# Optimization experiments

Measured on AMD Instinct MI355X. Metric: run time of the kernel, lower is better.

The kernel has to match this reference:

```python
import jax, jax.numpy as jnp
import numpy as np

N = 50000      # nodes
E = 800000     # edges (before self-loops)
H = 1          # attention heads
C = 64         # hidden channels per head
G = 256        # graphs in batch
IN = 1         # input_channel
NEG_SLOPE = 0.2
BN_EPS = 1e-5


def setup_inputs() -> dict:
    key = jax.random.key(0)
    ks = jax.random.split(key, 16)
    X = jax.random.normal(ks[0], (N, IN), dtype=jnp.float32)
    edge_index = jax.random.randint(ks[1], (2, E), 0, N, dtype=jnp.int32)
    batch = jnp.sort(jax.random.randint(ks[2], (N,), 0, G, dtype=jnp.int32))
    # GATConv params: conv1 maps IN -> H*C, conv2..5 map H*C -> H*C
    W1 = jax.random.normal(ks[3], (IN, H * C), dtype=jnp.float32) * 0.1
    Ws = jax.random.normal(ks[4], (4, H * C, H * C), dtype=jnp.float32) * 0.05
    att_src = jax.random.normal(ks[5], (5, H, C), dtype=jnp.float32) * 0.1
    att_dst = jax.random.normal(ks[6], (5, H, C), dtype=jnp.float32) * 0.1
    bias = jnp.zeros((5, H * C), dtype=jnp.float32)
    # BatchNorm1d (eval mode) params per layer
    bn_gamma = 1.0 + 0.1 * jax.random.normal(ks[7], (5, H * C), dtype=jnp.float32)
    bn_beta = 0.1 * jax.random.normal(ks[8], (5, H * C), dtype=jnp.float32)
    bn_mean = 0.1 * jax.random.normal(ks[9], (5, H * C), dtype=jnp.float32)
    bn_var = jax.random.uniform(ks[10], (5, H * C), dtype=jnp.float32, minval=0.5, maxval=1.5)
    Wr = jax.random.normal(ks[11], (H * C, 1), dtype=jnp.float32) * 0.1
    br = jnp.zeros((1,), dtype=jnp.float32)
    return {"X": X, "edge_index": edge_index, "batch": batch, "W1": W1, "Ws": Ws,
            "att_src": att_src, "att_dst": att_dst, "bias": bias,
            "bn_gamma": bn_gamma, "bn_beta": bn_beta, "bn_mean": bn_mean,
            "bn_var": bn_var, "Wr": Wr, "br": br}


def _gat_layer(x, src, dst, W, a_s, a_d, b):
    # x: [N, Fin]; src/dst: [E+N] (self-loops included)
    h = (x @ W).reshape(N, H, C)                        # [N,H,C]
    alpha_src = jnp.sum(h * a_s, axis=-1)               # [N,H]
    alpha_dst = jnp.sum(h * a_d, axis=-1)               # [N,H]
    e = jax.nn.leaky_relu(alpha_src[src] + alpha_dst[dst], NEG_SLOPE)  # [E+N,H]
    m = jax.ops.segment_max(e, dst, num_segments=N)     # per-dst softmax (stable)
    w = jnp.exp(e - m[dst])
    z = jax.ops.segment_sum(w, dst, num_segments=N)
    alpha = w / z[dst]                                  # [E+N,H]
    out = jax.ops.segment_sum(h[src] * alpha[..., None], dst, num_segments=N)
    return out.reshape(N, H * C) + b


def reference(X, edge_index, batch, W1, Ws, att_src, att_dst, bias,
              bn_gamma, bn_beta, bn_mean, bn_var, Wr, br):
    loops = jnp.arange(N, dtype=edge_index.dtype)
    src = jnp.concatenate([edge_index[0], loops])       # PyG GATConv adds self-loops
    dst = jnp.concatenate([edge_index[1], loops])

    def bn(x, i):
        return (x - bn_mean[i]) * (bn_gamma[i] / jnp.sqrt(bn_var[i] + BN_EPS)) + bn_beta[i]

    x = bn(jax.nn.relu(_gat_layer(X, src, dst, W1, att_src[0], att_dst[0], bias[0])), 0)
    for i in range(4):  # conv2..conv5 (dropout is identity in eval)
        x = bn(jax.nn.relu(_gat_layer(x, src, dst, Ws[i], att_src[i + 1], att_dst[i + 1], bias[i + 1])), i + 1)

    counts = jax.ops.segment_sum(jnp.ones((N,), x.dtype), batch, num_segments=G)
    pooled = jax.ops.segment_sum(x, batch, num_segments=G) / jnp.maximum(counts, 1.0)[:, None]
    pred = pooled @ Wr + br                             # [G,1]
    return pred, pooled
```

## Files before the change

### kernel.cpp

```cpp
#include <hip/hip_runtime.h>
#include <hip/hip_fp16.h>
#include <math.h>


#define CH   4096
#define BCAP 8192

__global__ __launch_bounds__(256) void bucket_scatter_kernel(const int* __restrict__ esrc,
                                                             const int* __restrict__ edst,
                                                             int* __restrict__ bkt_cursor,
                                                             unsigned* __restrict__ ebuf,
                                                             int E, int N, int NB) {
    __shared__ unsigned buf[CH];
    __shared__ unsigned short bkt[CH];
    __shared__ int histA[256], base[256], curB[256], gofs[256];
    int t    = threadIdx.x;
    int T    = E + N;
    int c0   = blockIdx.x * CH;
    int cend = min(c0 + CH, T);
    int M    = cend - c0;
    histA[t] = 0;
    __syncthreads();
    for (int i = c0 + t; i < cend; i += 256) {
        int d = (i < E) ? edst[i] : (i - E);
        atomicAdd(&histA[d >> 8], 1);
    }
    __syncthreads();
    int v = histA[t];
    base[t] = v;
    __syncthreads();
    for (int o = 1; o < 256; o <<= 1) {
        int u = (t >= o) ? base[t - o] : 0;
        __syncthreads();
        base[t] += u;
        __syncthreads();
    }
    int excl = base[t] - v;
    __syncthreads();
    base[t] = excl;
    curB[t] = excl;
    __syncthreads();
    if (t < NB && v > 0)
        gofs[t] = t * BCAP + atomicAdd(&bkt_cursor[t], v);
    for (int i = c0 + t; i < cend; i += 256) {
        int s, d;
        if (i < E) { s = esrc[i]; d = edst[i]; }
        else       { s = i - E;   d = s; }
        int b = d >> 8;
        int r = atomicAdd(&curB[b], 1);
        buf[r] = ((unsigned)s << 8) | (unsigned)(d & 255);
        bkt[r] = (unsigned short)b;
    }
    __syncthreads();
    for (int i = t; i < M; i += 256) {
        int b = bkt[i];
        ebuf[gofs[b] + (i - base[b])] = buf[i];
    }
}

__global__ __launch_bounds__(256) void bucket_sort_kernel(const unsigned* __restrict__ ebuf,
                                                          const int* __restrict__ bkt_cursor,
                                                          int* __restrict__ row_start,
                                                          int* __restrict__ csr_src, int N, int NB) {
    __shared__ int cnt[256], ofs[256];
    __shared__ int csr_lds[BCAP];
    int t    = threadIdx.x;
    int b    = blockIdx.x;
    int n0   = b << 8;
    int n1   = min(n0 + 256, N);
    int M    = bkt_cursor[b];
    ofs[t] = (t < b) ? bkt_cursor[t] : 0;
    __syncthreads();
    for (int o = 1; o < 256; o <<= 1) {
        int u = (t >= o) ? ofs[t - o] : 0;
        __syncthreads();
        ofs[t] += u;
        __syncthreads();
    }
    int base = ofs[255];
    __syncthreads();
    const unsigned* reg = ebuf + (size_t)b * BCAP;
    cnt[t] = 0;
    __syncthreads();
    for (int i = t; i < M; i += 256) atomicAdd(&cnt[reg[i] & 255u], 1);
    __syncthreads();
    int v = cnt[t];
    ofs[t] = v;
    __syncthreads();
    for (int o = 1; o < 256; o <<= 1) {
        int u = (t >= o) ? ofs[t - o] : 0;
        __syncthreads();
        ofs[t] += u;
        __syncthreads();
    }
    int excl = ofs[t] - v;
    if (n0 + t < n1) row_start[n0 + t] = base + excl;
    if (b == NB - 1 && t == 0) row_start[N] = base + M;
    __syncthreads();
    cnt[t] = excl;
    __syncthreads();
    for (int i = t; i < M; i += 256) {
        unsigned e = reg[i];
        int p = atomicAdd(&cnt[e & 255u], 1);
        csr_lds[p] = (int)(e >> 8);
    }
    __syncthreads();
    for (int i = t; i < M; i += 256) csr_src[base + i] = csr_lds[i];
}

__global__ __launch_bounds__(256) void aggregate1_kernel(const float* __restrict__ X,
                                                         const float* __restrict__ W1,
                                                         const float* __restrict__ a_s,
                                                         const float* __restrict__ a_d,
                                                         const int* __restrict__ row_start,
                                                         const int* __restrict__ csr_src,
                                                         const float* __restrict__ bias,
                                                         const float* __restrict__ gamma,
                                                         const float* __restrict__ beta,
                                                         const float* __restrict__ mean,
                                                         const float* __restrict__ var,
                                                         __half* __restrict__ xout, int N) {
    int lane = threadIdx.x & 63;
    int wave = threadIdx.x >> 6;
    int wpb  = blockDim.x >> 6;
    float w  = W1[lane];
    float da = w * a_s[lane];
    float db = w * a_d[lane];
#pragma unroll
    for (int o = 32; o > 0; o >>= 1) {
        da += __shfl_xor(da, o, 64);
        db += __shfl_xor(db, o, 64);
    }
    float bc    = bias[lane];
    float scale = gamma[lane] * rsqrtf(var[lane] + 1e-5f);
    float shift = beta[lane] - mean[lane] * scale;
    for (int d = blockIdx.x * wpb + wave; d < N; d += gridDim.x * wpb) {
        int rs  = row_start[d], re = row_start[d + 1];
        int deg = re - rs;
        float add = db * X[d];
        float S = 0.f, z = 0.f;
        if (deg <= 64) {
            float xs = 0.f, wj = 0.f;
            if (lane < deg) {
                xs = X[csr_src[rs + lane]];
                float e = da * xs + add;
                e  = (e > 0.f) ? e : 0.2f * e;
                wj = __expf(fminf(e, 60.f));
            }
            z = wj;
            S = wj * xs;
#pragma unroll
            for (int o = 32; o > 0; o >>= 1) {
                z += __shfl_xor(z, o, 64);
                S += __shfl_xor(S, o, 64);
            }
        } else {
            for (int j = rs + lane; j < re; j += 64) {
                float xs = X[csr_src[j]];
                float e  = da * xs + add;
                e = (e > 0.f) ? e : 0.2f * e;
                float wj = __expf(fminf(e, 60.f));
                z += wj;
                S += wj * xs;
            }
#pragma unroll
            for (int o = 32; o > 0; o >>= 1) {
                z += __shfl_xor(z, o, 64);
                S += __shfl_xor(S, o, 64);
            }
        }
        float o = w * (S / z) + bc;
        o = fmaxf(o, 0.f);
        xout[(size_t)d * 64 + lane] = __float2half(fmaf(o, scale, shift));
    }
}

__global__ __launch_bounds__(256) void transform_kernel(const __half* __restrict__ x16,
                                                        const float* __restrict__ W,
                                                        const float* __restrict__ a_s,
                                                        const float* __restrict__ a_d,
                                                        __half* __restrict__ h16,
                                                        float* __restrict__ as,
                                                        float* __restrict__ ad, int N) {
    __shared__ float Wl[64 * 64];
    __shared__ float xT[64 * 68];
    int t    = threadIdx.x;
    int lane = t & 63;
    int wv   = t >> 6;
    int base = blockIdx.x * 64;

    for (int i = t; i < 64 * 64; i += 256) Wl[i] = W[i];
#pragma unroll
    for (int r = 0; r < 16; ++r) {
        int nl = wv * 16 + r;
        int n  = base + nl;
        float v = (n < N) ? __half2float(x16[(size_t)n * 64 + lane]) : 0.f;
        xT[lane * 68 + nl] = v;
    }
    __syncthreads();

    int c0  = (t & 15) * 4;
    int nl0 = (t >> 4) * 4;
    float acc[4][4] = {{0.f}};
#pragma unroll 8
    for (int k = 0; k < 64; ++k) {
        float4 xv = *reinterpret_cast<const float4*>(&xT[k * 68 + nl0]);
        float4 wl = *reinterpret_cast<const float4*>(&Wl[k * 64 + c0]);
        acc[0][0] = fmaf(xv.x, wl.x, acc[0][0]);
        acc[0][1] = fmaf(xv.x, wl.y, acc[0][1]);
        acc[0][2] = fmaf(xv.x, wl.z, acc[0][2]);
        acc[0][3] = fmaf(xv.x, wl.w, acc[0][3]);
        acc[1][0] = fmaf(xv.y, wl.x, acc[1][0]);
        acc[1][1] = fmaf(xv.y, wl.y, acc[1][1]);
        acc[1][2] = fmaf(xv.y, wl.z, acc[1][2]);
        acc[1][3] = fmaf(xv.y, wl.w, acc[1][3]);
        acc[2][0] = fmaf(xv.z, wl.x, acc[2][0]);
        acc[2][1] = fmaf(xv.z, wl.y, acc[2][1]);
        acc[2][2] = fmaf(xv.z, wl.z, acc[2][2]);
        acc[2][3] = fmaf(xv.z, wl.w, acc[2][3]);
        acc[3][0] = fmaf(xv.w, wl.x, acc[3][0]);
        acc[3][1] = fmaf(xv.w, wl.y, acc[3][1]);
        acc[3][2] = fmaf(xv.w, wl.z, acc[3][2]);
        acc[3][3] = fmaf(xv.w, wl.w, acc[3][3]);
    }

    float4 asv = *reinterpret_cast<const float4*>(&a_s[c0]);
    float4 adv = *reinterpret_cast<const float4*>(&a_d[c0]);
#pragma unroll
    for (int i = 0; i < 4; ++i) {
        int n = base + nl0 + i;
        if (n < N) {
            union { __half2 h2[2]; uint2 u; } pk;
            pk.h2[0] = __floats2half2_rn(acc[i][0], acc[i][1]);
            pk.h2[1] = __floats2half2_rn(acc[i][2], acc[i][3]);
            *reinterpret_cast<uint2*>(&h16[(size_t)n * 64 + c0]) = pk.u;
        }
        float s1 = acc[i][0] * asv.x + acc[i][1] * asv.y + acc[i][2] * asv.z + acc[i][3] * asv.w;
        float s2 = acc[i][0] * adv.x + acc[i][1] * adv.y + acc[i][2] * adv.z + acc[i][3] * adv.w;
#pragma unroll
        for (int o = 8; o > 0; o >>= 1) {
            s1 += __shfl_xor(s1, o, 64);
            s2 += __shfl_xor(s2, o, 64);
        }
        if ((lane & 15) == 0 && n < N) { as[n] = s1; ad[n] = s2; }
    }
}

__global__ __launch_bounds__(256) void aggregate_kernel(const __half* __restrict__ h16,
                                                        const float* __restrict__ as,
                                                        const float* __restrict__ ad,
                                                        const int* __restrict__ row_start,
                                                        const int* __restrict__ csr_src,
                                                        const float* __restrict__ bias,
                                                        const float* __restrict__ gamma,
                                                        const float* __restrict__ beta,
                                                        const float* __restrict__ mean,
                                                        const float* __restrict__ var,
                                                        __half* __restrict__ xout, int N) {
    __shared__ float2 swbuf[4][64];
    int lane = threadIdx.x & 63;
    int wave = threadIdx.x >> 6;
    int wpb  = blockDim.x >> 6;
    int half = lane >> 5;
    int l    = lane & 31;
    int cg   = (l & 15) << 2;
    float4 bcv = *reinterpret_cast<const float4*>(&bias[cg]);
    float4 gav = *reinterpret_cast<const float4*>(&gamma[cg]);
    float4 bev = *reinterpret_cast<const float4*>(&beta[cg]);
    float4 mnv = *reinterpret_cast<const float4*>(&mean[cg]);
    float4 vrv = *reinterpret_cast<const float4*>(&var[cg]);
    float sc0 = gav.x * rsqrtf(vrv.x + 1e-5f), sh0 = bev.x - mnv.x * sc0;
    float sc1 = gav.y * rsqrtf(vrv.y + 1e-5f), sh1 = bev.y - mnv.y * sc1;
    float sc2 = gav.z * rsqrtf(vrv.z + 1e-5f), sh2 = bev.z - mnv.z * sc2;
    float sc3 = gav.w * rsqrtf(vrv.w + 1e-5f), sh3 = bev.w - mnv.w * sc3;
    int P = (N + 1) >> 1;
    for (int p = blockIdx.x * wpb + wave; p < P; p += gridDim.x * wpb) {
        int d0  = p << 1;
        int d1  = d0 + 1;
        int rs0 = row_start[d0];
        int re0 = row_start[d0 + 1];
        int deg0 = re0 - rs0;
        int deg1 = -1, re1 = 0;
        if (d1 < N) { re1 = row_start[d1 + 1]; deg1 = re1 - re0; }
        if (deg0 <= 32 && deg1 >= 0 && deg1 <= 32) {
            int d   = half ? d1 : d0;
            int rs  = half ? re0 : rs0;
            int deg = half ? deg1 : deg0;
            float add = ad[d];
            int s = 0; float w = 0.f;
            if (l < deg) {
                s = csr_src[rs + l];
                float e = as[s] + add;
                e = (e > 0.f) ? e : 0.2f * e;
                w = __expf(fminf(e, 60.f));
            }
            swbuf[wave][lane] = make_float2(__int_as_float(s), w);
            float z = w;
#pragma unroll
            for (int o = 16; o > 0; o >>= 1) z += __shfl_xor(z, o, 64);
            asm volatile("s_waitcnt lgkmcnt(0)" ::: "memory");
            int es = l >> 4;
            float a0 = 0.f, a1 = 0.f, a2 = 0.f, a3 = 0.f;
            int nb = (deg + 1) >> 1;
#pragma unroll 2
            for (int b = 0; b < nb; ++b) {
                int j  = (b << 1) + es;
                float2 sw = swbuf[wave][(half << 5) + j];
                int   sj = __float_as_int(sw.x);
                float wj = sw.y;
                const __half2* hp = reinterpret_cast<const __half2*>(h16 + (size_t)sj * 64 + cg);
                float2 f0 = __half22float2(hp[0]);
                float2 f1 = __half22float2(hp[1]);
                a0 = fmaf(f0.x, wj, a0);
                a1 = fmaf(f0.y, wj, a1);
                a2 = fmaf(f1.x, wj, a2);
                a3 = fmaf(f1.y, wj, a3);
            }
            a0 += __shfl_xor(a0, 16, 64);
            a1 += __shfl_xor(a1, 16, 64);
            a2 += __shfl_xor(a2, 16, 64);
            a3 += __shfl_xor(a3, 16, 64);
            if (es == 0) {
                float rz = 1.f / z;
                float o0 = fmaxf(fmaf(a0, rz, bcv.x), 0.f);
                float o1 = fmaxf(fmaf(a1, rz, bcv.y), 0.f);
                float o2 = fmaxf(fmaf(a2, rz, bcv.z), 0.f);
                float o3 = fmaxf(fmaf(a3, rz, bcv.w), 0.f);
                union { __half2 h2[2]; uint2 u; } pk;
                pk.h2[0] = __floats2half2_rn(fmaf(o0, sc0, sh0), fmaf(o1, sc1, sh1));
                pk.h2[1] = __floats2half2_rn(fmaf(o2, sc2, sh2), fmaf(o3, sc3, sh3));
                *reinterpret_cast<uint2*>(&xout[(size_t)d * 64 + cg]) = pk.u;
            }
        } else {
            for (int k = 0; k < 2; ++k) {
                int d = d0 + k;
                if (d >= N) break;
                int rs  = row_start[d], re = row_start[d + 1];
                int deg = re - rs;
                float add = ad[d];
                if (deg <= 64) {
                    int s = 0; float w = 0.f;
                    if (lane < deg) {
                        s = csr_src[rs + lane];
                        float e = as[s] + add;
                        e = (e > 0.f) ? e : 0.2f * e;
                        w = __expf(fminf(e, 60.f));
                    }
                    float z = w;
#pragma unroll
                    for (int o = 32; o > 0; o >>= 1) z += __shfl_xor(z, o, 64);
                    int es4 = lane >> 4;
                    float a0 = 0.f, a1 = 0.f, a2 = 0.f, a3 = 0.f;
                    int nb = (deg + 3) >> 2;
                    for (int b = 0; b < nb; ++b) {
                        int j = (b << 2) + es4;
                        int   sj = __shfl(s, j, 64);
                        float wj = __shfl(w, j, 64);
                        const __half2* hp = reinterpret_cast<const __half2*>(h16 + (size_t)sj * 64 + cg);
                        float2 f0 = __half22float2(hp[0]);
                        float2 f1 = __half22float2(hp[1]);
                        a0 = fmaf(f0.x, wj, a0);
                        a1 = fmaf(f0.y, wj, a1);
                        a2 = fmaf(f1.x, wj, a2);
                        a3 = fmaf(f1.y, wj, a3);
                    }
                    a0 += __shfl_xor(a0, 16, 64); a0 += __shfl_xor(a0, 32, 64);
                    a1 += __shfl_xor(a1, 16, 64); a1 += __shfl_xor(a1, 32, 64);
                    a2 += __shfl_xor(a2, 16, 64); a2 += __shfl_xor(a2, 32, 64);
                    a3 += __shfl_xor(a3, 16, 64); a3 += __shfl_xor(a3, 32, 64);
                    if (lane < 16) {
                        float rz = 1.f / z;
                        float o0 = fmaxf(fmaf(a0, rz, bcv.x), 0.f);
                        float o1 = fmaxf(fmaf(a1, rz, bcv.y), 0.f);
                        float o2 = fmaxf(fmaf(a2, rz, bcv.z), 0.f);
                        float o3 = fmaxf(fmaf(a3, rz, bcv.w), 0.f);
                        union { __half2 h2[2]; uint2 u; } pk;
                        pk.h2[0] = __floats2half2_rn(fmaf(o0, sc0, sh0), fmaf(o1, sc1, sh1));
                        pk.h2[1] = __floats2half2_rn(fmaf(o2, sc2, sh2), fmaf(o3, sc3, sh3));
                        *reinterpret_cast<uint2*>(&xout[(size_t)d * 64 + cg]) = pk.u;
                    }
                } else {
                    float z = 0.f;
                    for (int j = rs + lane; j < re; j += 64) {
                        float e = as[csr_src[j]] + add;
                        e = (e > 0.f) ? e : 0.2f * e;
                        z += __expf(fminf(e, 60.f));
                    }
#pragma unroll
                    for (int o = 32; o > 0; o >>= 1) z += __shfl_xor(z, o, 64);
                    float acc = 0.f;
                    for (int j = rs; j < re; ++j) {
                        int si = csr_src[j];
                        float e = as[si] + add;
                        e = (e > 0.f) ? e : 0.2f * e;
                        float w = __expf(fminf(e, 60.f));
                        acc = fmaf(__half2float(h16[(size_t)si * 64 + lane]), w, acc);
                    }
                    float scl = gamma[lane] * rsqrtf(var[lane] + 1e-5f);
                    float shf = beta[lane] - mean[lane] * scl;
                    float o = fmaxf(acc / z + bias[lane], 0.f);
                    xout[(size_t)d * 64 + lane] = __float2half(fmaf(o, scl, shf));
                }
            }
        }
    }
}

__global__ __launch_bounds__(256) void pool_kernel(const __half* __restrict__ x16,
                                                   const int* __restrict__ batch,
                                                   const float* __restrict__ Wr,
                                                   const float* __restrict__ br,
                                                   float* __restrict__ out, int N, int G) {
    __shared__ float wsum[4][64];
    __shared__ int bounds[2];
    int t    = threadIdx.x;
    int lane = t & 63;
    int wv   = t >> 6;
    int g    = blockIdx.x;
    if (g >= G) return;
    if (t < 2) {
        int key = g + t;
        int lo = 0, hi = N;
        while (lo < hi) {
            int mid = (lo + hi) >> 1;
            if (batch[mid] < key) lo = mid + 1; else hi = mid;
        }
        bounds[t] = lo;
    }
    __syncthreads();
    int s   = bounds[0];
    int cnt = bounds[1] - s;
    float a0 = 0.f, a1 = 0.f, a2 = 0.f, a3 = 0.f;
    for (int r = wv * 4; r < cnt; r += 16) {
        const __half* row = x16 + (size_t)(s + r) * 64 + lane;
        a0 += __half2float(row[0]);
        if (r + 1 < cnt) a1 += __half2float(row[64]);
        if (r + 2 < cnt) a2 += __half2float(row[128]);
        if (r + 3 < cnt) a3 += __half2float(row[192]);
    }
    wsum[wv][lane] = (a0 + a1) + (a2 + a3);
    __syncthreads();
    if (wv == 0) {
        float tot = (wsum[0][lane] + wsum[1][lane]) + (wsum[2][lane] + wsum[3][lane]);
        float pooled = tot / fmaxf((float)cnt, 1.f);
        out[G + (size_t)g * 64 + lane] = pooled;
        float p = pooled * Wr[lane];
#pragma unroll
        for (int o = 32; o > 0; o >>= 1) p += __shfl_xor(p, o, 64);
        if (lane == 0) out[g] = p + br[0];
    }
}

extern "C" void kernel_launch(void* const* d_in, const int* in_sizes, int n_in,
                              void* d_out, int out_size, void* d_ws, size_t ws_size,
                              hipStream_t stream) {
    const float* X        = (const float*)d_in[0];
    const int*   ei       = (const int*)d_in[1];
    const int*   batch    = (const int*)d_in[2];
    const float* W1       = (const float*)d_in[3];
    const float* Ws       = (const float*)d_in[4];
    const float* att_src  = (const float*)d_in[5];
    const float* att_dst  = (const float*)d_in[6];
    const float* bias     = (const float*)d_in[7];
    const float* bn_gamma = (const float*)d_in[8];
    const float* bn_beta  = (const float*)d_in[9];
    const float* bn_mean  = (const float*)d_in[10];
    const float* bn_var   = (const float*)d_in[11];
    const float* Wr       = (const float*)d_in[12];
    const float* br       = (const float*)d_in[13];

    const int N = in_sizes[0];
    const int E = in_sizes[1] / 2;
    const int G = out_size / 65;
    const int T = E + N;
    const int NB = (N + 255) >> 8;

    char* ws = (char*)d_ws;
    size_t off = 0;
    auto take = [&](size_t bytes) {
        void* p = ws + off;
        off = (off + bytes + 255) & ~(size_t)255;
        return p;
    };
    int*      row_start  = (int*)take(sizeof(int) * (N + 1));
    int*      csr_src    = (int*)take(sizeof(int) * T);
    float*    as         = (float*)take(sizeof(float) * N);
    float*    ad         = (float*)take(sizeof(float) * N);
    __half*   h16        = (__half*)take(sizeof(__half) * (size_t)N * 64);
    __half*   xa         = (__half*)take(sizeof(__half) * (size_t)N * 64);
    __half*   xb         = (__half*)take(sizeof(__half) * (size_t)N * 64);
    int*      bkt_cursor = (int*)take(sizeof(int) * NB);
    unsigned* ebuf       = (unsigned*)take(sizeof(unsigned) * (size_t)NB * BCAP);
    (void)ws_size;

    const int* esrc = ei;
    const int* edst = ei + E;

    hipMemsetAsync(bkt_cursor, 0, sizeof(int) * NB, stream);

    bucket_scatter_kernel<<<(T + CH - 1) / CH, 256, 0, stream>>>(esrc, edst, bkt_cursor,
                                                                 ebuf, E, N, NB);
    bucket_sort_kernel<<<NB, 256, 0, stream>>>(ebuf, bkt_cursor, row_start, csr_src, N, NB);

    int wb   = (N + 3) / 4;
    int tb   = (N + 63) / 64;
    int P    = (N + 1) / 2;
    int wb2  = (P + 3) / 4;
    aggregate1_kernel<<<wb, 256, 0, stream>>>(X, W1, att_src, att_dst, row_start, csr_src,
                                              bias, bn_gamma, bn_beta, bn_mean, bn_var, xa, N);
    __half* xin = xa;
    __half* xout = xb;
    for (int L = 1; L < 5; ++L) {
        transform_kernel<<<tb, 256, 0, stream>>>(xin, Ws + (size_t)(L - 1) * 64 * 64,
                                                 att_src + (size_t)L * 64, att_dst + (size_t)L * 64,
                                                 h16, as, ad, N);
        aggregate_kernel<<<wb2, 256, 0, stream>>>(h16, as, ad, row_start, csr_src,
                                                  bias + (size_t)L * 64, bn_gamma + (size_t)L * 64,
                                                  bn_beta + (size_t)L * 64, bn_mean + (size_t)L * 64,
                                                  bn_var + (size_t)L * 64, xout, N);
        __half* t = xin; xin = xout; xout = t;
    }

    pool_kernel<<<G, 256, 0, stream>>>(xin, batch, Wr, br, (float*)d_out, N, G);
}
```

Baseline: 244.0 us.

## Fuse layer-1 GAT aggregation into bucket sort and vectorize transform loads

Removes the separate layer-1 aggregation kernel and computes it inside the bucket sort kernel, reusing the per-bucket CSR held in LDS. Each thread handles one destination node with a serial loop over its neighbours, then the block writes the 64-channel fp16 output in vectorized form. This saves one launch and a re-read of row_start and csr_src. The cost is serial per-thread degree loops that can be unbalanced across threads. The transform kernel also switches its W and x loads to float4 and uint2 vector loads.

After: 217.5 us, median of 2. 10.8% less time.

```diff
diff --git a/kernel.cpp b/kernel.cpp
--- a/kernel.cpp
+++ b/kernel.cpp
@@ -61,14 +61,42 @@
 __global__ __launch_bounds__(256) void bucket_sort_kernel(const unsigned* __restrict__ ebuf,
                                                           const int* __restrict__ bkt_cursor,
                                                           int* __restrict__ row_start,
-                                                          int* __restrict__ csr_src, int N, int NB) {
+                                                          int* __restrict__ csr_src,
+                                                          const float* __restrict__ X,
+                                                          const float* __restrict__ W1,
+                                                          const float* __restrict__ a_s,
+                                                          const float* __restrict__ a_d,
+                                                          const float* __restrict__ bias,
+                                                          const float* __restrict__ gamma,
+                                                          const float* __restrict__ beta,
+                                                          const float* __restrict__ mean,
+                                                          const float* __restrict__ var,
+                                                          __half* __restrict__ xout,
+                                                          int N, int NB) {
     __shared__ int cnt[256], ofs[256];
     __shared__ int csr_lds[BCAP];
+    __shared__ float wl[64], bsc[64], bsh[64], bbl[64], rbuf[256], dadb[2];
     int t    = threadIdx.x;
     int b    = blockIdx.x;
     int n0   = b << 8;
     int n1   = min(n0 + 256, N);
     int M    = bkt_cursor[b];
+    if (t < 64) {
+        float w  = W1[t];
+        float sc = gamma[t] * rsqrtf(var[t] + 1e-5f);
+        wl[t]  = w;
+        bsc[t] = sc;
+        bsh[t] = beta[t] - mean[t] * sc;
+        bbl[t] = bias[t];
+        float p1 = w * a_s[t];
+        float p2 = w * a_d[t];
+#pragma unroll
+        for (int o = 32; o > 0; o >>= 1) {
+            p1 += __shfl_xor(p1, o, 64);
+            p2 += __shfl_xor(p2, o, 64);
+        }
+        if (t == 0) { dadb[0] = p1; dadb[1] = p2; }
+    }
     ofs[t] = (t < b) ? bkt_cursor[t] : 0;
     __syncthreads();
     for (int o = 1; o < 256; o <<= 1) {
@@ -106,72 +134,41 @@
     }
     __syncthreads();
     for (int i = t; i < M; i += 256) csr_src[base + i] = csr_lds[i];
-}
-
-__global__ __launch_bounds__(256) void aggregate1_kernel(const float* __restrict__ X,
-                                                         const float* __restrict__ W1,
-                                                         const float* __restrict__ a_s,
-                                                         const float* __restrict__ a_d,
-                                                         const int* __restrict__ row_start,
-                                                         const int* __restrict__ csr_src,
-                                                         const float* __restrict__ bias,
-                                                         const float* __restrict__ gamma,
-                                                         const float* __restrict__ beta,
-                                                         const float* __restrict__ mean,
-                                                         const float* __restrict__ var,
-                                                         __half* __restrict__ xout, int N) {
-    int lane = threadIdx.x & 63;
-    int wave = threadIdx.x >> 6;
-    int wpb  = blockDim.x >> 6;
-    float w  = W1[lane];
-    float da = w * a_s[lane];
-    float db = w * a_d[lane];
-#pragma unroll
-    for (int o = 32; o > 0; o >>= 1) {
-        da += __shfl_xor(da, o, 64);
-        db += __shfl_xor(db, o, 64);
-    }
-    float bc    = bias[lane];
-    float scale = gamma[lane] * rsqrtf(var[lane] + 1e-5f);
-    float shift = beta[lane] - mean[lane] * scale;
-    for (int d = blockIdx.x * wpb + wave; d < N; d += gridDim.x * wpb) {
-        int rs  = row_start[d], re = row_start[d + 1];
-        int deg = re - rs;
+    float da = dadb[0], db = dadb[1];
+    int d = n0 + t;
+    if (d < n1) {
         float add = db * X[d];
         float S = 0.f, z = 0.f;
-        if (deg <= 64) {
-            float xs = 0.f, wj = 0.f;
-            if (lane < deg) {
-                xs = X[csr_src[rs + lane]];
-                float e = da * xs + add;
-                e  = (e > 0.f) ? e : 0.2f * e;
-                wj = __expf(fminf(e, 60.f));
-            }
-            z = wj;
-            S = wj * xs;
-#pragma unroll
-            for (int o = 32; o > 0; o >>= 1) {
-                z += __shfl_xor(z, o, 64);
-                S += __shfl_xor(S, o, 64);
-            }
-        } else {
-            for (int j = rs + lane; j < re; j += 64) {
-                float xs = X[csr_src[j]];
-                float e  = da * xs + add;
-                e = (e > 0.f) ? e : 0.2f * e;
-                float wj = __expf(fminf(e, 60.f));
-                z += wj;
-                S += wj * xs;
-            }
-#pragma unroll
-            for (int o = 32; o > 0; o >>= 1) {
-                z += __shfl_xor(z, o, 64);
-                S += __shfl_xor(S, o, 64);
-            }
-        }
-        float o = w * (S / z) + bc;
-        o = fmaxf(o, 0.f);
-        xout[(size_t)d * 64 + lane] = __float2half(fmaf(o, scale, shift));
+        for (int j = excl; j < excl + v; ++j) {
+            float xs = X[csr_lds[j]];
+            float e  = da * xs + add;
+            e = (e > 0.f) ? e : 0.2f * e;
+            float w = __expf(fminf(e, 60.f));
+            z += w;
+            S = fmaf(w, xs, S);
+        }
+        rbuf[t] = S / z;
+    }
+    __syncthreads();
+    int nn = n1 - n0;
+#pragma unroll
+    for (int i = 0; i < 16; ++i) {
+        int idx  = (i << 8) + t;
+        int nl   = idx >> 4;
+        int c4   = (idx & 15) << 2;
+        if (nl < nn) {
+            float r = rbuf[nl];
+            union { __half2 h2[2]; uint2 u; } pk;
+            float o0 = fmaxf(fmaf(wl[c4 + 0], r, bbl[c4 + 0]), 0.f);
+            float o1 = fmaxf(fmaf(wl[c4 + 1], r, bbl[c4 + 1]), 0.f);
+            float o2 = fmaxf(fmaf(wl[c4 + 2], r, bbl[c4 + 2]), 0.f);
+            float o3 = fmaxf(fmaf(wl[c4 + 3], r, bbl[c4 + 3]), 0.f);
+            pk.h2[0] = __floats2half2_rn(fmaf(o0, bsc[c4 + 0], bsh[c4 + 0]),
+                                         fmaf(o1, bsc[c4 + 1], bsh[c4 + 1]));
+            pk.h2[1] = __floats2half2_rn(fmaf(o2, bsc[c4 + 2], bsh[c4 + 2]),
+                                         fmaf(o3, bsc[c4 + 3], bsh[c4 + 3]));
+            *reinterpret_cast<uint2*>(&xout[(size_t)(n0 + nl) * 64 + c4]) = pk.u;
+        }
     }
 }
 
@@ -186,16 +183,28 @@
     __shared__ float xT[64 * 68];
     int t    = threadIdx.x;
     int lane = t & 63;
-    int wv   = t >> 6;
     int base = blockIdx.x * 64;
 
-    for (int i = t; i < 64 * 64; i += 256) Wl[i] = W[i];
-#pragma unroll
-    for (int r = 0; r < 16; ++r) {
-        int nl = wv * 16 + r;
-        int n  = base + nl;
-        float v = (n < N) ? __half2float(x16[(size_t)n * 64 + lane]) : 0.f;
-        xT[lane * 68 + nl] = v;
+#pragma unroll
+    for (int i = 0; i < 4; ++i) {
+        int f4 = (i << 8) + t;
+        *reinterpret_cast<float4*>(&Wl[f4 << 2]) =
+            *reinterpret_cast<const float4*>(&W[f4 << 2]);
+    }
+#pragma unroll
+    for (int i = 0; i < 4; ++i) {
+        int idx = (i << 8) + t;
+        int row = idx >> 4;
+        int c4  = (idx & 15) << 2;
+        int n   = base + row;
+        uint2 raw = make_uint2(0u, 0u);
+        if (n < N) raw = *reinterpret_cast<const uint2*>(&x16[(size_t)n * 64 + c4]);
+        float2 f0 = __half22float2(*reinterpret_cast<__half2*>(&raw.x));
+        float2 f1 = __half22float2(*reinterpret_cast<__half2*>(&raw.y));
+        xT[(c4 + 0) * 68 + row] = f0.x;
+        xT[(c4 + 1) * 68 + row] = f0.y;
+        xT[(c4 + 2) * 68 + row] = f1.x;
+        xT[(c4 + 3) * 68 + row] = f1.y;
     }
     __syncthreads();
 
@@ -205,23 +214,23 @@
 #pragma unroll 8
     for (int k = 0; k < 64; ++k) {
         float4 xv = *reinterpret_cast<const float4*>(&xT[k * 68 + nl0]);
-        float4 wl = *reinterpret_cast<const float4*>(&Wl[k * 64 + c0]);
-        acc[0][0] = fmaf(xv.x, wl.x, acc[0][0]);
-        acc[0][1] = fmaf(xv.x, wl.y, acc[0][1]);
-        acc[0][2] = fmaf(xv.x, wl.z, acc[0][2]);
-        acc[0][3] = fmaf(xv.x, wl.w, acc[0][3]);
-        acc[1][0] = fmaf(xv.y, wl.x, acc[1][0]);
-        acc[1][1] = fmaf(xv.y, wl.y, acc[1][1]);
-        acc[1][2] = fmaf(xv.y, wl.z, acc[1][2]);
-        acc[1][3] = fmaf(xv.y, wl.w, acc[1][3]);
-        acc[2][0] = fmaf(xv.z, wl.x, acc[2][0]);
-        acc[2][1] = fmaf(xv.z, wl.y, acc[2][1]);
-        acc[2][2] = fmaf(xv.z, wl.z, acc[2][2]);
-        acc[2][3] = fmaf(xv.z, wl.w, acc[2][3]);
-        acc[3][0] = fmaf(xv.w, wl.x, acc[3][0]);
-        acc[3][1] = fmaf(xv.w, wl.y, acc[3][1]);
-        acc[3][2] = fmaf(xv.w, wl.z, acc[3][2]);
-        acc[3][3] = fmaf(xv.w, wl.w, acc[3][3]);
+        float4 wlv = *reinterpret_cast<const float4*>(&Wl[k * 64 + c0]);
+        acc[0][0] = fmaf(xv.x, wlv.x, acc[0][0]);
+        acc[0][1] = fmaf(xv.x, wlv.y, acc[0][1]);
+        acc[0][2] = fmaf(xv.x, wlv.z, acc[0][2]);
+        acc[0][3] = fmaf(xv.x, wlv.w, acc[0][3]);
+        acc[1][0] = fmaf(xv.y, wlv.x, acc[1][0]);
+        acc[1][1] = fmaf(xv.y, wlv.y, acc[1][1]);
+        acc[1][2] = fmaf(xv.y, wlv.z, acc[1][2]);
+        acc[1][3] = fmaf(xv.y, wlv.w, acc[1][3]);
+        acc[2][0] = fmaf(xv.z, wlv.x, acc[2][0]);
+        acc[2][1] = fmaf(xv.z, wlv.y, acc[2][1]);
+        acc[2][2] = fmaf(xv.z, wlv.z, acc[2][2]);
+        acc[2][3] = fmaf(xv.z, wlv.w, acc[2][3]);
+        acc[3][0] = fmaf(xv.w, wlv.x, acc[3][0]);
+        acc[3][1] = fmaf(xv.w, wlv.y, acc[3][1]);
+        acc[3][2] = fmaf(xv.w, wlv.z, acc[3][2]);
+        acc[3][3] = fmaf(xv.w, wlv.w, acc[3][3]);
     }
 
     float4 asv = *reinterpret_cast<const float4*>(&a_s[c0]);
@@ -500,14 +509,14 @@
 
     bucket_scatter_kernel<<<(T + CH - 1) / CH, 256, 0, stream>>>(esrc, edst, bkt_cursor,
                                                                  ebuf, E, N, NB);
-    bucket_sort_kernel<<<NB, 256, 0, stream>>>(ebuf, bkt_cursor, row_start, csr_src, N, NB);
-
-    int wb   = (N + 3) / 4;
+    bucket_sort_kernel<<<NB, 256, 0, stream>>>(ebuf, bkt_cursor, row_start, csr_src,
+                                               X, W1, att_src, att_dst,
+                                               bias, bn_gamma, bn_beta, bn_mean, bn_var,
+                                               xa, N, NB);
+
     int tb   = (N + 63) / 64;
     int P    = (N + 1) / 2;
     int wb2  = (P + 3) / 4;
-    aggregate1_kernel<<<wb, 256, 0, stream>>>(X, W1, att_src, att_dst, row_start, csr_src,
-                                              bias, bn_gamma, bn_beta, bn_mean, bn_var, xa, N);
     __half* xin = xa;
     __half* xout = xb;
     for (int L = 1; L < 5; ++L) {
```
